# Kernel optimization log

Measured on AMD Instinct MI355X. Metric: run time of the kernel, lower is better.

Reference implementation:

```python
import jax, jax.numpy as jnp
import numpy as np

B, L, DM = 4, 1024, 2048
H, KV, HD = 32, 4, 128
G = H // KV
E, TOPK, MI = 16, 8, 128
EPS = 1e-6
THETA = 1e6


def rms_norm(x, w):
    return x * jax.lax.rsqrt(jnp.mean(x * x, axis=-1, keepdims=True) + EPS) * w


def rotate_half(x):
    x1, x2 = jnp.split(x, 2, axis=-1)
    return jnp.concatenate([-x2, x1], axis=-1)


def setup_inputs() -> dict:
    key = jax.random.key(0)
    ks = jax.random.split(key, 10)
    s = 0.02
    # RoPE tables: [L, HD] broadcast to [B, L, HD]
    inv_freq = 1.0 / (THETA ** (jnp.arange(0, HD, 2, dtype=jnp.float32) / HD))
    ang = jnp.arange(L, dtype=jnp.float32)[:, None] * inv_freq[None, :]
    emb = jnp.concatenate([ang, ang], axis=-1)
    cos = jnp.broadcast_to(jnp.cos(emb)[None], (B, L, HD)).astype(jnp.float32)
    sin = jnp.broadcast_to(jnp.sin(emb)[None], (B, L, HD)).astype(jnp.float32)
    return {
        "x": jax.random.normal(ks[0], (B, L, DM), jnp.float32),
        "cos": cos,
        "sin": sin,
        "norm_attn_w": jnp.ones((DM,), jnp.float32),
        "q_w": jax.random.normal(ks[1], (H * HD, DM), jnp.float32) * s,
        "k_w": jax.random.normal(ks[2], (KV * HD, DM), jnp.float32) * s,
        "v_w": jax.random.normal(ks[3], (KV * HD, DM), jnp.float32) * s,
        "qn_w": jnp.ones((HD,), jnp.float32),
        "kn_w": jnp.ones((HD,), jnp.float32),
        "o_w": jax.random.normal(ks[4], (DM, H * HD), jnp.float32) * s,
        "norm_mlp_w": jnp.ones((DM,), jnp.float32),
        "router_w": jax.random.normal(ks[5], (E, DM), jnp.float32) * s,
        "egw": jax.random.normal(ks[6], (E, MI, DM), jnp.float32) * s,
        "euw": jax.random.normal(ks[7], (E, MI, DM), jnp.float32) * s,
        "edw": jax.random.normal(ks[8], (E, DM, MI), jnp.float32) * s,
    }


def _layer(x, cos, sin, norm_attn_w, q_w, k_w, v_w, qn_w, kn_w, o_w,
           norm_mlp_w, router_w, egw, euw, edw):
    b, l, dm = x.shape
    # ---- attention sub-block ----
    h = rms_norm(x, norm_attn_w)
    q = rms_norm((h @ q_w.T).reshape(b, l, H, HD), qn_w).swapaxes(1, 2)   # [B,H,L,D]
    k = rms_norm((h @ k_w.T).reshape(b, l, KV, HD), kn_w).swapaxes(1, 2)  # [B,KV,L,D]
    v = (h @ v_w.T).reshape(b, l, KV, HD).swapaxes(1, 2)                  # [B,KV,L,D]
    c = cos[:, None]  # [B,1,L,D]
    s = sin[:, None]
    q = c * q + s * rotate_half(q)
    k = c * k + s * rotate_half(k)
    # GQA: repeat kv heads
    k = jnp.repeat(k, G, axis=1)  # [B,H,L,D]
    v = jnp.repeat(v, G, axis=1)
    scores = jnp.einsum("bhqd,bhkd->bhqk", q, k) / jnp.sqrt(jnp.float32(HD))
    causal = jnp.tril(jnp.ones((l, l), bool))
    scores = jnp.where(causal[None, None], scores, jnp.float32(-1e30))
    attn = jax.nn.softmax(scores, axis=-1)
    o = jnp.einsum("bhqk,bhkd->bhqd", attn, v).swapaxes(1, 2).reshape(b, l, H * HD)
    x = x + o @ o_w.T
    # ---- sparse MoE MLP ----
    hm = rms_norm(x, norm_mlp_w).reshape(b * l, dm)  # [N,DM]
    logits = hm @ router_w.T                          # [N,E]
    probs = jax.nn.softmax(logits.astype(jnp.float32), axis=-1)
    rw, sel = jax.lax.top_k(probs, TOPK)              # [N,TOPK]
    rw = (rw / rw.sum(axis=-1, keepdims=True)).astype(x.dtype)
    n = b * l
    # dense combine weights [N,E] (topk indices are unique per token)
    w_dense = jnp.zeros((n, E), x.dtype).at[jnp.arange(n)[:, None], sel].add(rw)

    def body(acc, inp):
        gw, uw, dw, we = inp  # gw/uw [MI,DM], dw [DM,MI], we [N]
        a = jax.nn.silu(hm @ gw.T) * (hm @ uw.T)      # [N,MI]
        return acc + (a @ dw.T) * we[:, None], None

    out, _ = jax.lax.scan(body, jnp.zeros_like(hm), (egw, euw, edw, w_dense.T))
    return x + out.reshape(b, l, dm)


def reference(x, cos, sin, norm_attn_w, q_w, k_w, v_w, qn_w, kn_w, o_w,
              norm_mlp_w, router_w, egw, euw, edw):
    return _layer(x, cos, sin, norm_attn_w, q_w, k_w, v_w, qn_w, kn_w, o_w,
                  norm_mlp_w, router_w, egw, euw, edw)
```

## Files before the change

kernel.cpp:

```cpp
#include <hip/hip_runtime.h>
#include <stdint.h>

typedef _Float16 f16x8 __attribute__((ext_vector_type(8)));
typedef _Float16 f16x4 __attribute__((ext_vector_type(4)));
typedef float    f32x4 __attribute__((ext_vector_type(4)));

__device__ __forceinline__ void load16_lds(const _Float16* g, _Float16* l) {
    __builtin_amdgcn_global_load_lds(
        (const __attribute__((address_space(1))) void*)g,
        (__attribute__((address_space(3))) void*)l, 16, 0, 0);
}


__global__ void k_cast(const float* __restrict__ in, _Float16* __restrict__ out, int n) {
    int i = (blockIdx.x * 256 + threadIdx.x) * 4;
    if (i < n) {
        float4 v = *reinterpret_cast<const float4*>(in + i);
        f16x4 o = { (_Float16)v.x, (_Float16)v.y, (_Float16)v.z, (_Float16)v.w };
        *reinterpret_cast<f16x4*>(out + i) = o;
    }
}

__global__ void k_cast_dw(const float* __restrict__ edw, _Float16* __restrict__ dwc) {
    int t = blockIdx.x * 256 + threadIdx.x;
    int mi4 = (t & 31) * 4;
    int dm = (t >> 5) & 2047;
    int e = t >> 16;
    float4 v = *reinterpret_cast<const float4*>(edw + (((size_t)e * 2048 + dm) << 7) + mi4);
    f16x4 o = { (_Float16)v.x, (_Float16)v.y, (_Float16)v.z, (_Float16)v.w };
    *reinterpret_cast<f16x4*>(dwc + ((size_t)dm << 11) + e * 128 + mi4) = o;
}

__global__ __launch_bounds__(256) void k_rmsnorm(
    const float* __restrict__ x, const float* __restrict__ w,
    _Float16* __restrict__ oh, float* __restrict__ of)
{
    const int row = blockIdx.x, tid = threadIdx.x;
    const float* xr = x + (size_t)row * 2048;
    float4 a = *reinterpret_cast<const float4*>(xr + tid * 8);
    float4 b = *reinterpret_cast<const float4*>(xr + tid * 8 + 4);
    float ss = a.x*a.x + a.y*a.y + a.z*a.z + a.w*a.w
             + b.x*b.x + b.y*b.y + b.z*b.z + b.w*b.w;
    #pragma unroll
    for (int m = 1; m < 64; m <<= 1) ss += __shfl_xor(ss, m);
    __shared__ float red[4];
    if ((tid & 63) == 0) red[tid >> 6] = ss;
    __syncthreads();
    float tot = red[0] + red[1] + red[2] + red[3];
    float r = rsqrtf(tot * (1.f / 2048.f) + 1e-6f);
    float4 wa = *reinterpret_cast<const float4*>(w + tid * 8);
    float4 wb = *reinterpret_cast<const float4*>(w + tid * 8 + 4);
    float o0 = a.x*r*wa.x, o1 = a.y*r*wa.y, o2 = a.z*r*wa.z, o3 = a.w*r*wa.w;
    float o4 = b.x*r*wb.x, o5 = b.y*r*wb.y, o6 = b.z*r*wb.z, o7 = b.w*r*wb.w;
    f16x8 hv = { (_Float16)o0,(_Float16)o1,(_Float16)o2,(_Float16)o3,
                 (_Float16)o4,(_Float16)o5,(_Float16)o6,(_Float16)o7 };
    *reinterpret_cast<f16x8*>(oh + (size_t)row * 2048 + tid * 8) = hv;
    if (of) {
        float4 f0 = { o0, o1, o2, o3 }, f1 = { o4, o5, o6, o7 };
        *reinterpret_cast<float4*>(of + (size_t)row * 2048 + tid * 8) = f0;
        *reinterpret_cast<float4*>(of + (size_t)row * 2048 + tid * 8 + 4) = f1;
    }
}

__global__ __launch_bounds__(256) void k_gemm(
    const _Float16* __restrict__ A, int lda,
    const _Float16* __restrict__ W, int ldw,
    float* __restrict__ Cf, _Float16* __restrict__ Ch, int ldc,
    const float* __restrict__ resid, int K)
{
    __shared__ __align__(16) _Float16 As[3][128][32];
    __shared__ __align__(16) _Float16 Ws[3][128][32];
    const int r0 = blockIdx.x * 128, c0 = blockIdx.y * 128;
    const int tid = threadIdx.x, lane = tid & 63, wid = tid >> 6;
    const int wr = wid >> 1, wc = wid & 1;
    const int sr = lane >> 2;
    const int scs = ((lane & 3) ^ ((lane >> 3) & 3)) * 8;
    const int fr = lane & 15;
    const int rks = (((lane >> 4) ^ ((fr >> 1) & 3))) * 8;
    const f32x4 z4 = { 0.f, 0.f, 0.f, 0.f };
    f32x4 acc[4][4];
    #pragma unroll
    for (int i = 0; i < 4; i++)
        #pragma unroll
        for (int j = 0; j < 4; j++) acc[i][j] = z4;

    auto stage = [&](int bf, int k0) {
        #pragma unroll
        for (int i = 0; i < 2; i++) {
            int chunk = wid * 2 + i;
            load16_lds(A + (size_t)(r0 + chunk * 16 + sr) * lda + k0 + scs, &As[bf][chunk * 16][0]);
            load16_lds(W + (size_t)(c0 + chunk * 16 + sr) * ldw + k0 + scs, &Ws[bf][chunk * 16][0]);
        }
    };

    const int nt = K >> 5;
    stage(0, 0);
    if (nt > 1) stage(1, 32);
    int cur = 0;
    for (int t = 0; t < nt; t++) {
        if (t < nt - 1) asm volatile("s_waitcnt vmcnt(4)" ::: "memory");
        else            asm volatile("s_waitcnt vmcnt(0)" ::: "memory");
        __builtin_amdgcn_s_barrier();
        f16x8 af[4], bf4[4];
        #pragma unroll
        for (int i = 0; i < 4; i++)
            af[i] = *reinterpret_cast<const f16x8*>(&As[cur][wr * 64 + i * 16 + fr][rks]);
        #pragma unroll
        for (int j = 0; j < 4; j++)
            bf4[j] = *reinterpret_cast<const f16x8*>(&Ws[cur][wc * 64 + j * 16 + fr][rks]);
        if (t + 2 < nt) stage((t + 2) % 3, (t + 2) << 5);
        #pragma unroll
        for (int i = 0; i < 4; i++)
            #pragma unroll
            for (int j = 0; j < 4; j++)
                acc[i][j] = __builtin_amdgcn_mfma_f32_16x16x32_f16(af[i], bf4[j], acc[i][j], 0, 0, 0);
        cur = (cur + 1) % 3;
    }
    #pragma unroll
    for (int i = 0; i < 4; i++) {
        const int rowb = r0 + wr * 64 + i * 16 + (lane >> 4) * 4;
        #pragma unroll
        for (int j = 0; j < 4; j++) {
            const int col = c0 + wc * 64 + j * 16 + fr;
            #pragma unroll
            for (int r = 0; r < 4; r++) {
                size_t idx = (size_t)(rowb + r) * ldc + col;
                float v = acc[i][j][r];
                if (resid) v += resid[idx];
                if (Ch) Ch[idx] = (_Float16)v;
                else    Cf[idx] = v;
            }
        }
    }
}

__global__ __launch_bounds__(256) void k_qkv_post(
    const _Float16* __restrict__ qkv,
    const float* __restrict__ cosb, const float* __restrict__ sinb,
    const float* __restrict__ qn_w, const float* __restrict__ kn_w,
    _Float16* __restrict__ qh, _Float16* __restrict__ kh)
{
    const int tok = blockIdx.x;
    const int u = blockIdx.y * 4 + (threadIdx.x >> 6);
    const int lane = threadIdx.x & 63;
    const int b = tok >> 10, l = tok & 1023;
    const float c0 = cosb[(size_t)tok * 128 + lane];
    const float c1 = cosb[(size_t)tok * 128 + lane + 64];
    const float s0 = sinb[(size_t)tok * 128 + lane];
    const float s1 = sinb[(size_t)tok * 128 + lane + 64];
    if (u < 32) {
        const _Float16* base = qkv + (size_t)tok * 5120 + u * 128;
        float v0 = (float)base[lane], v1 = (float)base[lane + 64];
        float ss = v0 * v0 + v1 * v1;
        #pragma unroll
        for (int m = 1; m < 64; m <<= 1) ss += __shfl_xor(ss, m);
        float rms = rsqrtf(ss * (1.f / 128.f) + 1e-6f);
        float n0 = v0 * rms * qn_w[lane], n1 = v1 * rms * qn_w[lane + 64];
        _Float16* o = qh + (size_t)tok * 4096 + u * 128;
        o[lane]      = (_Float16)(c0 * n0 - s0 * n1);
        o[lane + 64] = (_Float16)(c1 * n1 + s1 * n0);
    } else {
        const int kvh = u - 32;
        const _Float16* base = qkv + (size_t)tok * 5120 + 4096 + kvh * 128;
        float v0 = (float)base[lane], v1 = (float)base[lane + 64];
        float ss = v0 * v0 + v1 * v1;
        #pragma unroll
        for (int m = 1; m < 64; m <<= 1) ss += __shfl_xor(ss, m);
        float rms = rsqrtf(ss * (1.f / 128.f) + 1e-6f);
        float n0 = v0 * rms * kn_w[lane], n1 = v1 * rms * kn_w[lane + 64];
        _Float16* o = kh + (((size_t)(b * 4 + kvh)) * 1024 + l) * 128;
        o[lane]      = (_Float16)(c0 * n0 - s0 * n1);
        o[lane + 64] = (_Float16)(c1 * n1 + s1 * n0);
    }
}

__global__ __launch_bounds__(256) void k_vt(
    const _Float16* __restrict__ qkv, _Float16* __restrict__ vth)
{
    const int bkv = blockIdx.x;
    const int b = bkv >> 2, kv = bkv & 3;
    const int l0 = blockIdx.y * 64, d0 = blockIdx.z * 64;
    __shared__ _Float16 T[64][72];
    const int t = threadIdx.x;
    const int r = t >> 3, c8 = (t & 7) * 8;
    #pragma unroll
    for (int rr = 0; rr < 2; rr++) {
        int l = l0 + r + rr * 32;
        *reinterpret_cast<f16x8*>(&T[r + rr * 32][c8]) =
            *reinterpret_cast<const f16x8*>(
                qkv + (size_t)(b * 1024 + l) * 5120 + 4608 + kv * 128 + d0 + c8);
    }
    __syncthreads();
    #pragma unroll
    for (int rr = 0; rr < 2; rr++) {
        int d = d0 + r + rr * 32;
        f16x8 v;
        #pragma unroll
        for (int j = 0; j < 8; j++) v[j] = T[c8 + j][r + rr * 32];
        *reinterpret_cast<f16x8*>(vth + ((size_t)(bkv * 128 + d)) * 1024 + l0 + c8) = v;
    }
}

__global__ __launch_bounds__(256) void k_attn(
    const _Float16* __restrict__ qh, const _Float16* __restrict__ kh,
    const _Float16* __restrict__ vth, _Float16* __restrict__ oh)
{
    const int bh = blockIdx.x;
    const int g = 15 - blockIdx.y;
    const int b = bh >> 5, h = bh & 31, kv = h >> 3;
    const int tid = threadIdx.x, lane = tid & 63, wid = tid >> 6;
    const int fr = lane & 15, fg = lane >> 4;
    const int q0w = g * 64 + wid * 16;

    __shared__ __align__(16) _Float16 Ks[64][128];
    __shared__ __align__(16) _Float16 Vs[128][64];
    __shared__ __align__(16) _Float16 Ps[4][16][72];

    const _Float16* kb = kh + ((size_t)(b * 4 + kv)) * 1024 * 128;
    const _Float16* vb = vth + ((size_t)(b * 4 + kv)) * 128 * 1024;

    f16x8 aq[4];
    {
        const _Float16* qbase = qh + ((size_t)(b * 1024 + q0w + fr)) * 4096 + h * 128;
        #pragma unroll
        for (int kk = 0; kk < 4; kk++)
            aq[kk] = *reinterpret_cast<const f16x8*>(qbase + kk * 32 + fg * 8);
    }

    float m_r[4] = { -1e30f, -1e30f, -1e30f, -1e30f };
    float l_r[4] = { 0.f, 0.f, 0.f, 0.f };
    const f32x4 z4 = { 0.f, 0.f, 0.f, 0.f };
    f32x4 oacc[8];
    #pragma unroll
    for (int dj = 0; dj < 8; dj++) oacc[dj] = z4;

    const int ntiles = g + 1;
    for (int kt = 0; kt < ntiles; kt++) {
        const int key0 = kt * 64;
        #pragma unroll
        for (int i = 0; i < 4; i++) {
            int rr = 16 * wid + 4 * i + (lane >> 4);
            int c16 = (lane & 15) ^ (rr & 7);
            load16_lds(kb + (size_t)(key0 + rr) * 128 + c16 * 8,
                       &Ks[0][0] + (16 * wid + 4 * i) * 128);
        }
        #pragma unroll
        for (int i = 0; i < 4; i++) {
            int rr = 32 * wid + 8 * i + (lane >> 3);
            int c16 = (lane & 7) ^ (rr & 7);
            load16_lds(vb + (size_t)rr * 1024 + key0 + c16 * 8,
                       &Vs[0][0] + (32 * wid + 8 * i) * 64);
        }
        __syncthreads();

        f32x4 sc[4];
        #pragma unroll
        for (int j = 0; j < 4; j++) sc[j] = z4;
        #pragma unroll
        for (int j = 0; j < 4; j++) {
            #pragma unroll
            for (int kk = 0; kk < 4; kk++) {
                f16x8 bk = *reinterpret_cast<const f16x8*>(
                    &Ks[0][0] + (j * 16 + fr) * 128 + (((kk * 4 + fg) ^ (fr & 7)) * 8));
                sc[j] = __builtin_amdgcn_mfma_f32_16x16x32_f16(aq[kk], bk, sc[j], 0, 0, 0);
            }
        }

        const bool lastt = (kt == ntiles - 1);
        float pmax[4] = { -1e30f, -1e30f, -1e30f, -1e30f };
        #pragma unroll
        for (int j = 0; j < 4; j++) {
            const int key = key0 + j * 16 + fr;
            #pragma unroll
            for (int r = 0; r < 4; r++) {
                float v = sc[j][r] * 0.08838834764831845f;
                if (lastt && key > q0w + fg * 4 + r) v = -1e30f;
                sc[j][r] = v;
                pmax[r] = fmaxf(pmax[r], v);
            }
        }
        #pragma unroll
        for (int m = 1; m < 16; m <<= 1)
            #pragma unroll
            for (int r = 0; r < 4; r++) pmax[r] = fmaxf(pmax[r], __shfl_xor(pmax[r], m));
        float alpha[4];
        #pragma unroll
        for (int r = 0; r < 4; r++) {
            float mn = fmaxf(m_r[r], pmax[r]);
            alpha[r] = __expf(m_r[r] - mn);
            m_r[r] = mn;
        }
        float rs[4] = { 0.f, 0.f, 0.f, 0.f };
        #pragma unroll
        for (int j = 0; j < 4; j++)
            #pragma unroll
            for (int r = 0; r < 4; r++) {
                float p = __expf(sc[j][r] - m_r[r]);
                sc[j][r] = p;
                rs[r] += p;
            }
        #pragma unroll
        for (int m = 1; m < 16; m <<= 1)
            #pragma unroll
            for (int r = 0; r < 4; r++) rs[r] += __shfl_xor(rs[r], m);
        #pragma unroll
        for (int r = 0; r < 4; r++) l_r[r] = l_r[r] * alpha[r] + rs[r];
        #pragma unroll
        for (int dj = 0; dj < 8; dj++)
            #pragma unroll
            for (int r = 0; r < 4; r++) oacc[dj][r] *= alpha[r];

        #pragma unroll
        for (int j = 0; j < 4; j++)
            #pragma unroll
            for (int r = 0; r < 4; r++)
                Ps[wid][fg * 4 + r][j * 16 + fr] = (_Float16)sc[j][r];

        #pragma unroll
        for (int ks = 0; ks < 2; ks++) {
            f16x8 ap = *reinterpret_cast<const f16x8*>(&Ps[wid][fr][ks * 32 + fg * 8]);
            #pragma unroll
            for (int dj = 0; dj < 8; dj++) {
                f16x8 bv = *reinterpret_cast<const f16x8*>(
                    &Vs[0][0] + (dj * 16 + fr) * 64 + (((ks * 4 + fg) ^ (fr & 7)) * 8));
                oacc[dj] = __builtin_amdgcn_mfma_f32_16x16x32_f16(ap, bv, oacc[dj], 0, 0, 0);
            }
        }
        __syncthreads();
    }

    float inv[4];
    #pragma unroll
    for (int r = 0; r < 4; r++) inv[r] = 1.f / l_r[r];
    #pragma unroll
    for (int dj = 0; dj < 8; dj++)
        #pragma unroll
        for (int r = 0; r < 4; r++)
            oh[((size_t)(b * 1024 + q0w + fg * 4 + r)) * 4096 + h * 128 + dj * 16 + fr] =
                (_Float16)(oacc[dj][r] * inv[r]);
}

__global__ __launch_bounds__(256) void k_router(
    const float* __restrict__ hm, const float* __restrict__ rw,
    float* __restrict__ wdense)
{
    const int tok = blockIdx.x * 4 + (threadIdx.x >> 6);
    const int lane = threadIdx.x & 63;
    __shared__ float lg[4][16];
    const float* hr = hm + (size_t)tok * 2048;
    for (int e = 0; e < 16; e++) {
        float acc = 0.f;
        #pragma unroll
        for (int i = 0; i < 32; i++) acc += hr[i * 64 + lane] * rw[(size_t)e * 2048 + i * 64 + lane];
        #pragma unroll
        for (int m = 1; m < 64; m <<= 1) acc += __shfl_xor(acc, m);
        if (lane == 0) lg[threadIdx.x >> 6][e] = acc;
    }
    __syncthreads();
    if (lane == 0) {
        float* l = lg[threadIdx.x >> 6];
        float mx = l[0];
        for (int e = 1; e < 16; e++) mx = fmaxf(mx, l[e]);
        float p[16]; float sum = 0.f;
        for (int e = 0; e < 16; e++) { p[e] = expf(l[e] - mx); sum += p[e]; }
        for (int e = 0; e < 16; e++) p[e] /= sum;
        bool sel[16]; for (int e = 0; e < 16; e++) sel[e] = false;
        float ssum = 0.f;
        for (int t = 0; t < 8; t++) {
            int bi = -1; float bv = -1.f;
            for (int e = 0; e < 16; e++) if (!sel[e] && p[e] > bv) { bv = p[e]; bi = e; }
            sel[bi] = true; ssum += bv;
        }
        for (int e = 0; e < 16; e++)
            wdense[(size_t)e * 4096 + tok] = sel[e] ? p[e] / ssum : 0.f;
    }
}

__global__ __launch_bounds__(256) void k_moe_gu(
    const _Float16* __restrict__ hm, const _Float16* __restrict__ gw,
    const _Float16* __restrict__ uw, const float* __restrict__ wdense,
    _Float16* __restrict__ ab)
{
    const int r0 = blockIdx.x * 128, e = blockIdx.y;
    const _Float16* G = gw + (size_t)e * 128 * 2048;
    const _Float16* U = uw + (size_t)e * 128 * 2048;
    __shared__ __align__(16) _Float16 As[2][128][32];
    __shared__ __align__(16) _Float16 Gs[2][128][32];
    __shared__ __align__(16) _Float16 Us[2][128][32];
    const int tid = threadIdx.x, lane = tid & 63, wid = tid >> 6;
    const int wr = wid >> 1, wc = wid & 1;
    const int sr = lane >> 2;
    const int scs = ((lane & 3) ^ ((lane >> 3) & 3)) * 8;
    const int fr = lane & 15;
    const int rks = (((lane >> 4) ^ ((fr >> 1) & 3))) * 8;
    const f32x4 z4 = { 0.f, 0.f, 0.f, 0.f };
    f32x4 ag[4][4], au[4][4];
    #pragma unroll
    for (int i = 0; i < 4; i++)
        #pragma unroll
        for (int j = 0; j < 4; j++) { ag[i][j] = z4; au[i][j] = z4; }

    auto stage = [&](int bf, int k0) {
        #pragma unroll
        for (int i = 0; i < 2; i++) {
            int chunk = wid * 2 + i;
            load16_lds(hm + (size_t)(r0 + chunk * 16 + sr) * 2048 + k0 + scs, &As[bf][chunk * 16][0]);
            load16_lds(G + (size_t)(chunk * 16 + sr) * 2048 + k0 + scs, &Gs[bf][chunk * 16][0]);
            load16_lds(U + (size_t)(chunk * 16 + sr) * 2048 + k0 + scs, &Us[bf][chunk * 16][0]);
        }
    };

    stage(0, 0);
    __syncthreads();
    int cur = 0;
    for (int t = 0; t < 64; t++) {
        if (t + 1 < 64) stage(cur ^ 1, (t + 1) << 5);
        f16x8 af[4], bg[4], bu[4];
        #pragma unroll
        for (int i = 0; i < 4; i++)
            af[i] = *reinterpret_cast<const f16x8*>(&As[cur][wr * 64 + i * 16 + fr][rks]);
        #pragma unroll
        for (int j = 0; j < 4; j++) {
            bg[j] = *reinterpret_cast<const f16x8*>(&Gs[cur][wc * 64 + j * 16 + fr][rks]);
            bu[j] = *reinterpret_cast<const f16x8*>(&Us[cur][wc * 64 + j * 16 + fr][rks]);
        }
        #pragma unroll
        for (int i = 0; i < 4; i++)
            #pragma unroll
            for (int j = 0; j < 4; j++) {
                ag[i][j] = __builtin_amdgcn_mfma_f32_16x16x32_f16(af[i], bg[j], ag[i][j], 0, 0, 0);
                au[i][j] = __builtin_amdgcn_mfma_f32_16x16x32_f16(af[i], bu[j], au[i][j], 0, 0, 0);
            }
        __syncthreads();
        cur ^= 1;
    }
    #pragma unroll
    for (int i = 0; i < 4; i++) {
        const int rowb = r0 + wr * 64 + i * 16 + (lane >> 4) * 4;
        float wv[4];
        #pragma unroll
        for (int r = 0; r < 4; r++) wv[r] = wdense[(size_t)e * 4096 + rowb + r];
        #pragma unroll
        for (int j = 0; j < 4; j++) {
            const int col = e * 128 + wc * 64 + j * 16 + fr;
            #pragma unroll
            for (int r = 0; r < 4; r++) {
                float g = ag[i][j][r], uu = au[i][j][r];
                float sil = g / (1.f + __expf(-g));
                ab[(size_t)(rowb + r) * 2048 + col] = (_Float16)(sil * uu * wv[r]);
            }
        }
    }
}


extern "C" void kernel_launch(void* const* d_in, const int* in_sizes, int n_in,
                              void* d_out, int out_size, void* d_ws, size_t ws_size,
                              hipStream_t stream)
{
    const float* x        = (const float*)d_in[0];
    const float* cosb     = (const float*)d_in[1];
    const float* sinb     = (const float*)d_in[2];
    const float* nattn    = (const float*)d_in[3];
    const float* q_w      = (const float*)d_in[4];
    const float* k_w      = (const float*)d_in[5];
    const float* v_w      = (const float*)d_in[6];
    const float* qn_w     = (const float*)d_in[7];
    const float* kn_w     = (const float*)d_in[8];
    const float* o_w      = (const float*)d_in[9];
    const float* nmlp     = (const float*)d_in[10];
    const float* router_w = (const float*)d_in[11];
    const float* egw      = (const float*)d_in[12];
    const float* euw      = (const float*)d_in[13];
    const float* edw      = (const float*)d_in[14];

    char* w = (char*)d_ws;
    _Float16* qkvw_h = (_Float16*)(w + 0);
    _Float16* ow_h   = (_Float16*)(w + 20971520);
    _Float16* gw_h   = (_Float16*)(w + 37748736);
    _Float16* uw_h   = (_Float16*)(w + 46137344);
    _Float16* dwc_h  = (_Float16*)(w + 54525952);
    _Float16* h_h    = (_Float16*)(w + 62914560);
    _Float16* hm_h   = h_h;
    float*    x2     = (float*)(w + 79691776);
    _Float16* qkv_h  = (_Float16*)(w + 113246208);
    _Float16* o_h    = qkv_h;
    _Float16* ab_h   = qkv_h;
    _Float16* q_h    = (_Float16*)(w + 155189248);
    float*    hm_f   = (float*)(w + 155189248);
    _Float16* k_h    = (_Float16*)(w + 188743680);
    _Float16* vt_h   = (_Float16*)(w + 192937984);
    float*    wdense = (float*)(w + 197132288);

    k_cast<<<8192, 256, 0, stream>>>(q_w, qkvw_h, 8388608);
    k_cast<<<1024, 256, 0, stream>>>(k_w, qkvw_h + (size_t)4096 * 2048, 1048576);
    k_cast<<<1024, 256, 0, stream>>>(v_w, qkvw_h + (size_t)4608 * 2048, 1048576);
    k_cast<<<8192, 256, 0, stream>>>(o_w, ow_h, 8388608);
    k_cast<<<4096, 256, 0, stream>>>(egw, gw_h, 4194304);
    k_cast<<<4096, 256, 0, stream>>>(euw, uw_h, 4194304);
    k_cast_dw<<<4096, 256, 0, stream>>>(edw, dwc_h);

    k_rmsnorm<<<4096, 256, 0, stream>>>(x, nattn, h_h, nullptr);
    k_gemm<<<dim3(32, 40), 256, 0, stream>>>(h_h, 2048, qkvw_h, 2048,
                                             nullptr, qkv_h, 5120, nullptr, 2048);
    k_qkv_post<<<dim3(4096, 9), 256, 0, stream>>>(qkv_h, cosb, sinb, qn_w, kn_w, q_h, k_h);
    k_vt<<<dim3(16, 16, 2), 256, 0, stream>>>(qkv_h, vt_h);
    k_attn<<<dim3(128, 16), 256, 0, stream>>>(q_h, k_h, vt_h, o_h);
    k_gemm<<<dim3(32, 16), 256, 0, stream>>>(o_h, 4096, ow_h, 4096,
                                             x2, nullptr, 2048, x, 4096);
    k_rmsnorm<<<4096, 256, 0, stream>>>(x2, nmlp, hm_h, hm_f);
    k_router<<<1024, 256, 0, stream>>>(hm_f, router_w, wdense);
    k_moe_gu<<<dim3(32, 16), 256, 0, stream>>>(hm_h, gw_h, uw_h, wdense, ab_h);
    k_gemm<<<dim3(32, 16), 256, 0, stream>>>(ab_h, 2048, dwc_h, 2048,
                                             (float*)d_out, nullptr, 2048, x2, 2048);

    (void)in_sizes; (void)n_in; (void)out_size; (void)ws_size;
}
```

Before: 565.6 us.

## Add 128x256 GEMM kernel, interleave gate/up weights, split MoE SiLU combine

Adds a new GEMM kernel with a 128x256 output tile and one barrier per K step. It is used for the QKV projection and for a single combined gate+up projection, built from gate/up weights interleaved per expert. The fused MoE gate/up kernel is replaced by this GEMM plus a separate SiLU·up·route-weight combine kernel. The goal is better operand reuse and fewer barriers per MFMA. The cost is writing and re-reading a 4096x4096 fp16 intermediate and launching one extra kernel.

```diff
diff --git a/kernel.cpp b/kernel.cpp
--- a/kernel.cpp
+++ b/kernel.cpp
@@ -29,6 +29,21 @@
     float4 v = *reinterpret_cast<const float4*>(edw + (((size_t)e * 2048 + dm) << 7) + mi4);
     f16x4 o = { (_Float16)v.x, (_Float16)v.y, (_Float16)v.z, (_Float16)v.w };
     *reinterpret_cast<f16x4*>(dwc + ((size_t)dm << 11) + e * 128 + mi4) = o;
+}
+
+__global__ __launch_bounds__(256) void k_cast_guw(
+    const float* __restrict__ eg, const float* __restrict__ eu,
+    _Float16* __restrict__ out)
+{
+    const int row = blockIdx.x;
+    const int e = row >> 8, rem = row & 255, half = rem >> 7, mi = rem & 127;
+    const float* src = (half ? eu : eg) + ((size_t)(e * 128 + mi)) * 2048;
+    const int c = threadIdx.x * 8;
+    float4 v0 = *reinterpret_cast<const float4*>(src + c);
+    float4 v1 = *reinterpret_cast<const float4*>(src + c + 4);
+    f16x8 o = { (_Float16)v0.x,(_Float16)v0.y,(_Float16)v0.z,(_Float16)v0.w,
+                (_Float16)v1.x,(_Float16)v1.y,(_Float16)v1.z,(_Float16)v1.w };
+    *reinterpret_cast<f16x8*>(out + (size_t)row * 2048 + c) = o;
 }
 
 __global__ __launch_bounds__(256) void k_rmsnorm(
@@ -134,6 +149,94 @@
     }
 }
 
+__global__ __launch_bounds__(256) void k_gemm2(
+    const _Float16* __restrict__ A, int lda,
+    const _Float16* __restrict__ W, int ldw,
+    _Float16* __restrict__ Ch, int ldc, int K)
+{
+    __shared__ __align__(16) _Float16 As[2][128][32];
+    __shared__ __align__(16) _Float16 Ws[2][256][32];
+    const int r0 = blockIdx.x * 128, c0 = blockIdx.y * 256;
+    const int tid = threadIdx.x, lane = tid & 63, wid = tid >> 6;
+    const int sr4 = lane >> 2;
+    const int scs = ((lane & 3) ^ ((lane >> 3) & 3)) * 8;
+    const int fr = lane & 15;
+    const int rks = (((lane >> 4) ^ ((fr >> 1) & 3))) * 8;
+    const f32x4 z4 = { 0.f, 0.f, 0.f, 0.f };
+    f32x4 acc[8][4];
+    #pragma unroll
+    for (int i = 0; i < 8; i++)
+        #pragma unroll
+        for (int j = 0; j < 4; j++) acc[i][j] = z4;
+
+    auto stage = [&](int bf, int k0) {
+        #pragma unroll
+        for (int i = 0; i < 2; i++) {
+            int rowb = wid * 32 + i * 16;
+            load16_lds(A + (size_t)(r0 + rowb + sr4) * lda + k0 + scs, &As[bf][rowb][0]);
+        }
+        #pragma unroll
+        for (int i = 0; i < 4; i++) {
+            int rowb = wid * 64 + i * 16;
+            load16_lds(W + (size_t)(c0 + rowb + sr4) * ldw + k0 + scs, &Ws[bf][rowb][0]);
+        }
+    };
+
+    const int nt = K >> 5;
+    stage(0, 0);
+    int cur = 0;
+    for (int t = 0; t < nt; t++) {
+        asm volatile("s_waitcnt vmcnt(0)" ::: "memory");
+        __builtin_amdgcn_s_barrier();
+        if (t + 1 < nt) stage(cur ^ 1, (t + 1) << 5);
+        f16x8 af[8], bf4[4];
+        #pragma unroll
+        for (int i = 0; i < 8; i++)
+            af[i] = *reinterpret_cast<const f16x8*>(&As[cur][i * 16 + fr][rks]);
+        #pragma unroll
+        for (int j = 0; j < 4; j++)
+            bf4[j] = *reinterpret_cast<const f16x8*>(&Ws[cur][wid * 64 + j * 16 + fr][rks]);
+        #pragma unroll
+        for (int i = 0; i < 8; i++)
+            #pragma unroll
+            for (int j = 0; j < 4; j++)
+                acc[i][j] = __builtin_amdgcn_mfma_f32_16x16x32_f16(af[i], bf4[j], acc[i][j], 0, 0, 0);
+        cur ^= 1;
+    }
+    #pragma unroll
+    for (int i = 0; i < 8; i++) {
+        const int rowb = r0 + i * 16 + (lane >> 4) * 4;
+        #pragma unroll
+        for (int j = 0; j < 4; j++) {
+            const int col = c0 + wid * 64 + j * 16 + fr;
+            #pragma unroll
+            for (int r = 0; r < 4; r++)
+                Ch[(size_t)(rowb + r) * ldc + col] = (_Float16)acc[i][j][r];
+        }
+    }
+}
+
+__global__ __launch_bounds__(256) void k_gu_comb(
+    const _Float16* __restrict__ gucat, const float* __restrict__ wdense,
+    _Float16* __restrict__ ab)
+{
+    const int tok = blockIdx.x;
+    const int idx = threadIdx.x;
+    const int e = idx >> 4, mi8 = (idx & 15) * 8;
+    const _Float16* gp = gucat + (size_t)tok * 4096 + e * 256 + mi8;
+    f16x8 gv = *reinterpret_cast<const f16x8*>(gp);
+    f16x8 uv = *reinterpret_cast<const f16x8*>(gp + 128);
+    float wv = wdense[(size_t)e * 4096 + tok];
+    f16x8 o;
+    #pragma unroll
+    for (int j = 0; j < 8; j++) {
+        float g = (float)gv[j], u = (float)uv[j];
+        float sil = g / (1.f + __expf(-g));
+        o[j] = (_Float16)(sil * u * wv);
+    }
+    *reinterpret_cast<f16x8*>(ab + (size_t)tok * 2048 + e * 128 + mi8) = o;
+}
+
 __global__ __launch_bounds__(256) void k_qkv_post(
     const _Float16* __restrict__ qkv,
     const float* __restrict__ cosb, const float* __restrict__ sinb,
@@ -373,83 +476,6 @@
         }
         for (int e = 0; e < 16; e++)
             wdense[(size_t)e * 4096 + tok] = sel[e] ? p[e] / ssum : 0.f;
-    }
-}
-
-__global__ __launch_bounds__(256) void k_moe_gu(
-    const _Float16* __restrict__ hm, const _Float16* __restrict__ gw,
-    const _Float16* __restrict__ uw, const float* __restrict__ wdense,
-    _Float16* __restrict__ ab)
-{
-    const int r0 = blockIdx.x * 128, e = blockIdx.y;
-    const _Float16* G = gw + (size_t)e * 128 * 2048;
-    const _Float16* U = uw + (size_t)e * 128 * 2048;
-    __shared__ __align__(16) _Float16 As[2][128][32];
-    __shared__ __align__(16) _Float16 Gs[2][128][32];
-    __shared__ __align__(16) _Float16 Us[2][128][32];
-    const int tid = threadIdx.x, lane = tid & 63, wid = tid >> 6;
-    const int wr = wid >> 1, wc = wid & 1;
-    const int sr = lane >> 2;
-    const int scs = ((lane & 3) ^ ((lane >> 3) & 3)) * 8;
-    const int fr = lane & 15;
-    const int rks = (((lane >> 4) ^ ((fr >> 1) & 3))) * 8;
-    const f32x4 z4 = { 0.f, 0.f, 0.f, 0.f };
-    f32x4 ag[4][4], au[4][4];
-    #pragma unroll
-    for (int i = 0; i < 4; i++)
-        #pragma unroll
-        for (int j = 0; j < 4; j++) { ag[i][j] = z4; au[i][j] = z4; }
-
-    auto stage = [&](int bf, int k0) {
-        #pragma unroll
-        for (int i = 0; i < 2; i++) {
-            int chunk = wid * 2 + i;
-            load16_lds(hm + (size_t)(r0 + chunk * 16 + sr) * 2048 + k0 + scs, &As[bf][chunk * 16][0]);
-            load16_lds(G + (size_t)(chunk * 16 + sr) * 2048 + k0 + scs, &Gs[bf][chunk * 16][0]);
-            load16_lds(U + (size_t)(chunk * 16 + sr) * 2048 + k0 + scs, &Us[bf][chunk * 16][0]);
-        }
-    };
-
-    stage(0, 0);
-    __syncthreads();
-    int cur = 0;
-    for (int t = 0; t < 64; t++) {
-        if (t + 1 < 64) stage(cur ^ 1, (t + 1) << 5);
-        f16x8 af[4], bg[4], bu[4];
-        #pragma unroll
-        for (int i = 0; i < 4; i++)
-            af[i] = *reinterpret_cast<const f16x8*>(&As[cur][wr * 64 + i * 16 + fr][rks]);
-        #pragma unroll
-        for (int j = 0; j < 4; j++) {
-            bg[j] = *reinterpret_cast<const f16x8*>(&Gs[cur][wc * 64 + j * 16 + fr][rks]);
-            bu[j] = *reinterpret_cast<const f16x8*>(&Us[cur][wc * 64 + j * 16 + fr][rks]);
-        }
-        #pragma unroll
-        for (int i = 0; i < 4; i++)
-            #pragma unroll
-            for (int j = 0; j < 4; j++) {
-                ag[i][j] = __builtin_amdgcn_mfma_f32_16x16x32_f16(af[i], bg[j], ag[i][j], 0, 0, 0);
-                au[i][j] = __builtin_amdgcn_mfma_f32_16x16x32_f16(af[i], bu[j], au[i][j], 0, 0, 0);
-            }
-        __syncthreads();
-        cur ^= 1;
-    }
-    #pragma unroll
-    for (int i = 0; i < 4; i++) {
-        const int rowb = r0 + wr * 64 + i * 16 + (lane >> 4) * 4;
-        float wv[4];
-        #pragma unroll
-        for (int r = 0; r < 4; r++) wv[r] = wdense[(size_t)e * 4096 + rowb + r];
-        #pragma unroll
-        for (int j = 0; j < 4; j++) {
-            const int col = e * 128 + wc * 64 + j * 16 + fr;
-            #pragma unroll
-            for (int r = 0; r < 4; r++) {
-                float g = ag[i][j][r], uu = au[i][j][r];
-                float sil = g / (1.f + __expf(-g));
-                ab[(size_t)(rowb + r) * 2048 + col] = (_Float16)(sil * uu * wv[r]);
-            }
-        }
     }
 }
 
@@ -477,8 +503,7 @@
     char* w = (char*)d_ws;
     _Float16* qkvw_h = (_Float16*)(w + 0);
     _Float16* ow_h   = (_Float16*)(w + 20971520);
-    _Float16* gw_h   = (_Float16*)(w + 37748736);
-    _Float16* uw_h   = (_Float16*)(w + 46137344);
+    _Float16* guw_h  = (_Float16*)(w + 37748736);
     _Float16* dwc_h  = (_Float16*)(w + 54525952);
     _Float16* h_h    = (_Float16*)(w + 62914560);
     _Float16* hm_h   = h_h;
@@ -488,6 +513,7 @@
     _Float16* ab_h   = qkv_h;
     _Float16* q_h    = (_Float16*)(w + 155189248);
     float*    hm_f   = (float*)(w + 155189248);
+    _Float16* gucat  = (_Float16*)(w + 155189248);
     _Float16* k_h    = (_Float16*)(w + 188743680);
     _Float16* vt_h   = (_Float16*)(w + 192937984);
     float*    wdense = (float*)(w + 197132288);
@@ -496,13 +522,11 @@
     k_cast<<<1024, 256, 0, stream>>>(k_w, qkvw_h + (size_t)4096 * 2048, 1048576);
     k_cast<<<1024, 256, 0, stream>>>(v_w, qkvw_h + (size_t)4608 * 2048, 1048576);
     k_cast<<<8192, 256, 0, stream>>>(o_w, ow_h, 8388608);
-    k_cast<<<4096, 256, 0, stream>>>(egw, gw_h, 4194304);
-    k_cast<<<4096, 256, 0, stream>>>(euw, uw_h, 4194304);
+    k_cast_guw<<<4096, 256, 0, stream>>>(egw, euw, guw_h);
     k_cast_dw<<<4096, 256, 0, stream>>>(edw, dwc_h);
 
     k_rmsnorm<<<4096, 256, 0, stream>>>(x, nattn, h_h, nullptr);
-    k_gemm<<<dim3(32, 40), 256, 0, stream>>>(h_h, 2048, qkvw_h, 2048,
-                                             nullptr, qkv_h, 5120, nullptr, 2048);
+    k_gemm2<<<dim3(32, 20), 256, 0, stream>>>(h_h, 2048, qkvw_h, 2048, qkv_h, 5120, 2048);
     k_qkv_post<<<dim3(4096, 9), 256, 0, stream>>>(qkv_h, cosb, sinb, qn_w, kn_w, q_h, k_h);
     k_vt<<<dim3(16, 16, 2), 256, 0, stream>>>(qkv_h, vt_h);
     k_attn<<<dim3(128, 16), 256, 0, stream>>>(q_h, k_h, vt_h, o_h);
@@ -510,7 +534,8 @@
                                              x2, nullptr, 2048, x, 4096);
     k_rmsnorm<<<4096, 256, 0, stream>>>(x2, nmlp, hm_h, hm_f);
     k_router<<<1024, 256, 0, stream>>>(hm_f, router_w, wdense);
-    k_moe_gu<<<dim3(32, 16), 256, 0, stream>>>(hm_h, gw_h, uw_h, wdense, ab_h);
+    k_gemm2<<<dim3(32, 16), 256, 0, stream>>>(hm_h, 2048, guw_h, 2048, gucat, 4096, 2048);
+    k_gu_comb<<<4096, 256, 0, stream>>>(gucat, wdense, ab_h);
     k_gemm<<<dim3(32, 16), 256, 0, stream>>>(ab_h, 2048, dwc_h, 2048,
                                              (float*)d_out, nullptr, 2048, x2, 2048);
 
```

Result: slower. 669.8 us (+18.4%).
